# Optimization experiments

Measured on AMD Instinct MI355X. Metric: run time of the kernel, lower is better.

Reference implementation:

```python
import jax, jax.numpy as jnp
import numpy as np

N_NODES = 100000
N_EDGES = 1200000
N_FEAT = 128
HIDDEN = 64
N_GRAPHS = 256


def setup_inputs() -> dict:
    key = jax.random.key(0)
    ks = jax.random.split(key, 8)
    x = jax.random.normal(ks[0], (N_NODES, N_FEAT), dtype=jnp.float32)
    edge_index = jax.random.randint(ks[1], (2, N_EDGES), 0, N_NODES, dtype=jnp.int64)
    batch = jnp.sort(jax.random.randint(ks[2], (N_NODES,), 0, N_GRAPHS, dtype=jnp.int64))
    W1 = jax.random.normal(ks[3], (N_FEAT, HIDDEN), dtype=jnp.float32) * (1.0 / np.sqrt(N_FEAT))
    b1 = jnp.zeros((HIDDEN,), dtype=jnp.float32)
    W2 = jax.random.normal(ks[4], (HIDDEN, HIDDEN), dtype=jnp.float32) * (1.0 / np.sqrt(HIDDEN))
    b2 = jnp.zeros((HIDDEN,), dtype=jnp.float32)
    Wl = jax.random.normal(ks[5], (HIDDEN, 1), dtype=jnp.float32) * (1.0 / np.sqrt(HIDDEN))
    bl = jnp.zeros((1,), dtype=jnp.float32)
    return {"x": x, "edge_index": edge_index, "batch": batch,
            "W1": W1, "b1": b1, "W2": W2, "b2": b2, "Wl": Wl, "bl": bl}


def _gcn_conv(x, src, dst, W, b, n):
    # PyG GCNConv: linear transform, then sym-normalized scatter-add (self-loops already in src/dst)
    h = x @ W  # [N, out]
    deg = jax.ops.segment_sum(jnp.ones(src.shape[0], x.dtype), dst, num_segments=n)
    dinv = jnp.where(deg > 0, jax.lax.rsqrt(deg), jnp.zeros_like(deg))
    norm = dinv[src] * dinv[dst]  # [E+N]
    out = jax.ops.segment_sum(norm[:, None] * h[src], dst, num_segments=n)
    return out + b


def reference(x, edge_index, batch, W1, b1, W2, b2, Wl, bl):
    n = x.shape[0]
    loops = jnp.arange(n, dtype=edge_index.dtype)
    src = jnp.concatenate([edge_index[0], loops])
    dst = jnp.concatenate([edge_index[1], loops])
    h = _gcn_conv(x, src, dst, W1, b1, n)
    h = jax.nn.relu(h)
    h = _gcn_conv(h, src, dst, W2, b2, n)
    # global mean pool over graphs
    sums = jax.ops.segment_sum(h, batch, num_segments=N_GRAPHS)
    cnts = jax.ops.segment_sum(jnp.ones((n,), h.dtype), batch, num_segments=N_GRAPHS)
    pooled = sums / jnp.maximum(cnts, 1.0)[:, None]
    return pooled @ Wl + bl
```

## Files before the change

### kernel.cpp

```cpp
#include <hip/hip_runtime.h>

#define N_NODES 100000
#define N_EDGES 1200000
#define R_BUCKETS 256
#define RSZ 400
#define CAP 8192
#define CH 4096
#define NC 293

typedef _Float16 h8 __attribute__((ext_vector_type(8)));
typedef _Float16 h2 __attribute__((ext_vector_type(2)));
typedef float f32x16 __attribute__((ext_vector_type(16)));

__global__ __launch_bounds__(256) void bkt_scatter(const int* __restrict__ src,
                                                   const int* __restrict__ dst,
                                                   int* __restrict__ bucket_alloc,
                                                   int* __restrict__ ebuf, int E) {
    __shared__ int h[R_BUCKETS];
    __shared__ int off[R_BUCKETS];
    h[threadIdx.x] = 0;
    __syncthreads();
    int e0 = blockIdx.x * CH;
    int e1 = min(e0 + CH, E);
    for (int e = e0 + (int)threadIdx.x; e < e1; e += 256)
        atomicAdd(&h[dst[e] / RSZ], 1);
    __syncthreads();
    int b = threadIdx.x;
    int hc = h[b];
    off[b] = b * CAP + (hc > 0 ? atomicAdd(&bucket_alloc[b], hc) : 0);
    __syncthreads();
    for (int e = e0 + (int)threadIdx.x; e < e1; e += 256) {
        int d = dst[e];
        int bk = d / RSZ;
        int p = atomicAdd(&off[bk], 1);
        ebuf[p] = (src[e] << 9) | (d - bk * RSZ);
    }
}

__global__ __launch_bounds__(256) void bkt_build(const int* __restrict__ ebuf,
                                                 const int* __restrict__ bcnt,
                                                 int2* __restrict__ row2,
                                                 float* __restrict__ dinv,
                                                 int* __restrict__ csr, int N) {
    __shared__ int hist[RSZ];
    __shared__ int pref[RSZ];
    __shared__ int part[256];
    int r = blockIdx.x;
    int nbase = r * RSZ;
    int ebase = r * CAP;
    int ecnt = bcnt[r];
    for (int i = threadIdx.x; i < RSZ; i += 256) hist[i] = 0;
    __syncthreads();
    for (int e = (int)threadIdx.x; e < ecnt; e += 256)
        atomicAdd(&hist[ebuf[ebase + e] & 511], 1);
    __syncthreads();
    for (int i = threadIdx.x; i < RSZ; i += 256) {
        int gi = nbase + i;
        if (gi < N) dinv[gi] = rsqrtf((float)hist[i] + 1.0f);
    }
    int s0 = threadIdx.x * 2;
    int sum = (s0 < RSZ) ? hist[s0] + hist[s0 + 1] : 0;
    part[threadIdx.x] = sum;
    __syncthreads();
    for (int off = 1; off < 256; off <<= 1) {
        int v = (threadIdx.x >= off) ? part[threadIdx.x - off] : 0;
        __syncthreads();
        part[threadIdx.x] += v;
        __syncthreads();
    }
    if (s0 < RSZ) {
        int run = part[threadIdx.x] - sum;
        pref[s0] = run;
        pref[s0 + 1] = run + hist[s0];
    }
    __syncthreads();
    for (int i = threadIdx.x; i < RSZ; i += 256) {
        int gi = nbase + i;
        if (gi < N) row2[gi] = make_int2(ebase + pref[i], ebase + pref[i] + hist[i]);
    }
    __syncthreads();
    for (int e = (int)threadIdx.x; e < ecnt; e += 256) {
        int epk = ebuf[ebase + e];
        int t = atomicAdd(&pref[epk & 511], 1);
        csr[ebase + t] = (int)(((unsigned)epk) >> 9);
    }
}

__global__ void prep_kernel(const float* __restrict__ W1, const float* __restrict__ W2,
                            const float* __restrict__ Wl, float* __restrict__ w2l,
                            _Float16* __restrict__ whi, _Float16* __restrict__ wlo) {
    if (blockIdx.x == 32) {
        if (threadIdx.x < 64) {
            int f = threadIdx.x;
            float s = 0.0f;
            for (int o = 0; o < 64; o++) s += W2[f * 64 + o] * Wl[o];
            w2l[f] = s;
        }
        return;
    }
    int idx = blockIdx.x * 256 + threadIdx.x;
    int j = idx & 7;
    int lane = (idx >> 3) & 63;
    int kk = (idx >> 9) & 7;
    int nt = idx >> 12;
    int k = kk * 16 + (lane >> 5) * 8 + j;
    int n = nt * 32 + (lane & 31);
    float v = W1[k * 64 + n];
    _Float16 hi = (_Float16)v;
    whi[idx] = hi;
    wlo[idx] = (_Float16)(v - (float)hi);
}

__global__ __launch_bounds__(256) void gemm_mfma(const float* __restrict__ x,
                                                 const _Float16* __restrict__ whi,
                                                 const _Float16* __restrict__ wlo,
                                                 const float* __restrict__ dinv,
                                                 _Float16* __restrict__ out, int N) {
    int wave = threadIdx.x >> 6;
    int lane = threadIdx.x & 63;
    int base = blockIdx.x * 128 + wave * 32;
    int row = base + (lane & 31);
    int rowc = min(row, N - 1);
    const float* xrow = x + (size_t)rowc * 128 + (lane >> 5) * 8;

    f32x16 acc0, acc1;
#pragma unroll
    for (int i = 0; i < 16; i++) { acc0[i] = 0.f; acc1[i] = 0.f; }

#pragma unroll
    for (int kk = 0; kk < 8; kk++) {
        float4 xa = *reinterpret_cast<const float4*>(xrow + kk * 16);
        float4 xb = *reinterpret_cast<const float4*>(xrow + kk * 16 + 4);
        float xv[8] = {xa.x, xa.y, xa.z, xa.w, xb.x, xb.y, xb.z, xb.w};
        h8 ahi, alo;
#pragma unroll
        for (int j = 0; j < 8; j++) {
            _Float16 hi = (_Float16)xv[j];
            ahi[j] = hi;
            alo[j] = (_Float16)(xv[j] - (float)hi);
        }
        h8 b0h = *reinterpret_cast<const h8*>(whi + (size_t)(kk * 64 + lane) * 8);
        h8 b0l = *reinterpret_cast<const h8*>(wlo + (size_t)(kk * 64 + lane) * 8);
        h8 b1h = *reinterpret_cast<const h8*>(whi + (size_t)((8 + kk) * 64 + lane) * 8);
        h8 b1l = *reinterpret_cast<const h8*>(wlo + (size_t)((8 + kk) * 64 + lane) * 8);
        acc0 = __builtin_amdgcn_mfma_f32_32x32x16_f16(ahi, b0h, acc0, 0, 0, 0);
        acc0 = __builtin_amdgcn_mfma_f32_32x32x16_f16(ahi, b0l, acc0, 0, 0, 0);
        acc0 = __builtin_amdgcn_mfma_f32_32x32x16_f16(alo, b0h, acc0, 0, 0, 0);
        acc1 = __builtin_amdgcn_mfma_f32_32x32x16_f16(ahi, b1h, acc1, 0, 0, 0);
        acc1 = __builtin_amdgcn_mfma_f32_32x32x16_f16(ahi, b1l, acc1, 0, 0, 0);
        acc1 = __builtin_amdgcn_mfma_f32_32x32x16_f16(alo, b1h, acc1, 0, 0, 0);
    }

    int col = lane & 31;
    int rbase = base + 4 * (lane >> 5);
#pragma unroll
    for (int reg = 0; reg < 16; reg++) {
        int node = rbase + (reg & 3) + 8 * (reg >> 2);
        if (node < N) {
            float di = dinv[node];
            out[(size_t)node * 64 + col] = (_Float16)(di * acc0[reg]);
            out[(size_t)node * 64 + 32 + col] = (_Float16)(di * acc1[reg]);
        }
    }
}

#define AGG_NPB 32
__global__ __launch_bounds__(256) void agg1_kernel(const _Float16* __restrict__ t,
                                                   const int2* __restrict__ row2,
                                                   const int* __restrict__ csr,
                                                   const float* __restrict__ dinv,
                                                   const float* __restrict__ b1,
                                                   const float* __restrict__ w2l,
                                                   float* __restrict__ q, int N) {
    int lane = threadIdx.x & 63;
    int w = threadIdx.x >> 6;
    int hl = lane & 31;
    int hsel = lane >> 5;
    float2 b1v = reinterpret_cast<const float2*>(b1)[hl];
    float2 wlv = reinterpret_cast<const float2*>(w2l)[hl];
    int i0 = blockIdx.x * AGG_NPB;
    int iend = min(i0 + AGG_NPB, N);
    for (int ip = i0 + 2 * w; ip < iend; ip += 8) {
        int iA = ip;
        int iB = ip + 1;
        bool hasB = iB < iend;
        int2 rrA = row2[iA];
        int2 rrB = hasB ? row2[iB] : make_int2(rrA.x, rrA.x);
        int myi = hsel ? iB : iA;
        int myic = min(myi, N - 1);
        int rs = hsel ? rrB.x : rrA.x;
        int re = hsel ? rrB.y : rrA.y;
        int deg = re - rs;
        int kmax = max(rrA.y - rrA.x, rrB.y - rrB.x);
        int rlast = max(re - 1, rs);
        h2 sv = *reinterpret_cast<const h2*>(t + ((size_t)myic << 6) + (hl << 1));
        float a0 = (float)sv[0];
        float a1 = (float)sv[1];
        for (int base = 0; base < kmax; base += 32) {
            int sp = min(csr[min(rs + base + hl, rlast)] & 0x1FFFF, N - 1);
            int kend = min(kmax - base, 32);
            {
                h2 vv[16];
#pragma unroll
                for (int j = 0; j < 16; j++) {
                    int s = __shfl(sp, j, 32);
                    vv[j] = *reinterpret_cast<const h2*>(t + ((size_t)s << 6) + (hl << 1));
                }
#pragma unroll
                for (int j = 0; j < 16; j++) {
                    if (base + j < deg) {
                        a0 += (float)vv[j][0];
                        a1 += (float)vv[j][1];
                    }
                }
            }
            if (kend > 16) {
                h2 vv[16];
#pragma unroll
                for (int j = 0; j < 16; j++) {
                    int s = __shfl(sp, 16 + j, 32);
                    vv[j] = *reinterpret_cast<const h2*>(t + ((size_t)s << 6) + (hl << 1));
                }
#pragma unroll
                for (int j = 0; j < 16; j++) {
                    if (base + 16 + j < deg) {
                        a0 += (float)vv[j][0];
                        a1 += (float)vv[j][1];
                    }
                }
            }
        }
        float di = dinv[myic];
        float h0 = fmaxf(di * a0 + b1v.x, 0.f);
        float h1 = fmaxf(di * a1 + b1v.y, 0.f);
        float p = h0 * wlv.x + h1 * wlv.y;
        p += __shfl_xor(p, 1, 64);
        p += __shfl_xor(p, 2, 64);
        p += __shfl_xor(p, 4, 64);
        p += __shfl_xor(p, 8, 64);
        p += __shfl_xor(p, 16, 64);
        if (hl == 0 && myi < iend) q[myi] = di * p;
    }
}

__global__ __launch_bounds__(256) void agg2_pool_kernel(const float* __restrict__ q,
                                                        const int2* __restrict__ row2,
                                                        const int* __restrict__ csr,
                                                        const float* __restrict__ dinv,
                                                        const int* __restrict__ batch,
                                                        float* __restrict__ gsum,
                                                        float* __restrict__ gcnt, int N) {
    __shared__ float bins[256];
    __shared__ float cbins[256];
    bins[threadIdx.x] = 0.0f;
    cbins[threadIdx.x] = 0.0f;
    __syncthreads();
    int i = blockIdx.x * 256 + threadIdx.x;
    if (i < N) {
        int2 rr = row2[i];
        int rs = rr.x, re = rr.y;
        float acc = q[i];
        int rl = max(re - 1, rs);
        for (int j = rs; j < re; j += 4) {
            int e0 = csr[j];
            int e1 = csr[min(j + 1, rl)];
            int e2 = csr[min(j + 2, rl)];
            int e3 = csr[min(j + 3, rl)];
            float v0 = q[e0];
            float v1 = q[e1];
            float v2 = q[e2];
            float v3 = q[e3];
            acc += v0;
            if (j + 1 < re) acc += v1;
            if (j + 2 < re) acc += v2;
            if (j + 3 < re) acc += v3;
        }
        int g = batch[i];
        atomicAdd(&bins[g], dinv[i] * acc);
        atomicAdd(&cbins[g], 1.0f);
    }
    __syncthreads();
    int i0 = blockIdx.x * 256;
    if (i0 < N) {
        int ilast = min(i0 + 255, N - 1);
        int gmin = batch[i0];
        int gmax = batch[ilast];
        for (int g = gmin + (int)threadIdx.x; g <= gmax; g += 256) {
            atomicAdd(&gsum[g], bins[g]);
            atomicAdd(&gcnt[g], cbins[g]);
        }
    }
}

__global__ void out_kernel(const float* __restrict__ gsum, const float* __restrict__ gcnt,
                           const float* __restrict__ b2, const float* __restrict__ Wl,
                           const float* __restrict__ bl, float* __restrict__ out) {
    int g = threadIdx.x;
    int lane = g & 63;
    float c = b2[lane] * Wl[lane];
    c += __shfl_xor(c, 1, 64);
    c += __shfl_xor(c, 2, 64);
    c += __shfl_xor(c, 4, 64);
    c += __shfl_xor(c, 8, 64);
    c += __shfl_xor(c, 16, 64);
    c += __shfl_xor(c, 32, 64);
    out[g] = gsum[g] / fmaxf(gcnt[g], 1.0f) + c + bl[0];
}

extern "C" void kernel_launch(void* const* d_in, const int* in_sizes, int n_in,
                              void* d_out, int out_size, void* d_ws, size_t ws_size,
                              hipStream_t stream) {
    const float* x  = (const float*)d_in[0];
    const int*   ei = (const int*)d_in[1];
    const int*   batch = (const int*)d_in[2];
    const float* W1 = (const float*)d_in[3];
    const float* b1 = (const float*)d_in[4];
    const float* W2 = (const float*)d_in[5];
    const float* b2 = (const float*)d_in[6];
    const float* Wl = (const float*)d_in[7];
    const float* bl = (const float*)d_in[8];
    float* out = (float*)d_out;

    const int N = N_NODES, E = N_EDGES;
    const int nblk = (N + 255) / 256;
    const int* src = ei;
    const int* dst = ei + E;

    char* ws = (char*)d_ws;
    int*      ebuf      = (int*)ws;       ws += (size_t)R_BUCKETS * CAP * 4;
    int*      csr       = (int*)ws;       ws += (size_t)R_BUCKETS * CAP * 4;
    _Float16* buf1      = (_Float16*)ws;  ws += 6400000 * 2;
    int2*     row2      = (int2*)ws;      ws += 100096 * 8;
    float*    dinv      = (float*)ws;     ws += 100096 * 4;
    float*    q         = (float*)ws;     ws += 100096 * 4;
    float*    gsum      = (float*)ws;     ws += 256 * 4;
    int*      bucket_alloc = (int*)ws;    ws += 256 * 4;
    float*    gcnt      = (float*)ws;     ws += 256 * 4;
    float*    w2l       = (float*)ws;     ws += 256 * 4;
    _Float16* whi       = (_Float16*)ws;  ws += 8192 * 2;
    _Float16* wlo       = (_Float16*)ws;  ws += 8192 * 2;

    hipMemsetAsync(gsum, 0, 3072, stream);

    bkt_scatter<<<NC, 256, 0, stream>>>(src, dst, bucket_alloc, ebuf, E);
    bkt_build<<<R_BUCKETS, 256, 0, stream>>>(ebuf, bucket_alloc, row2, dinv, csr, N);

    prep_kernel<<<33, 256, 0, stream>>>(W1, W2, Wl, w2l, whi, wlo);

    gemm_mfma<<<(N + 127) / 128, 256, 0, stream>>>(x, whi, wlo, dinv, buf1, N);

    agg1_kernel<<<(N + AGG_NPB - 1) / AGG_NPB, 256, 0, stream>>>(
        buf1, row2, csr, dinv, b1, w2l, q, N);

    agg2_pool_kernel<<<nblk, 256, 0, stream>>>(q, row2, csr, dinv, batch, gsum, gcnt, N);

    out_kernel<<<1, 256, 0, stream>>>(gsum, gcnt, b2, Wl, bl, out);
}
```

Measured before the change: 201.7 us.

## Fuse degree counting, weight prep and output finalize into neighboring kernels

```diff
diff --git a/kernel.cpp b/kernel.cpp
--- a/kernel.cpp
+++ b/kernel.cpp
@@ -12,35 +12,67 @@
 typedef _Float16 h2 __attribute__((ext_vector_type(2)));
 typedef float f32x16 __attribute__((ext_vector_type(16)));
 
-__global__ __launch_bounds__(256) void bkt_scatter(const int* __restrict__ src,
-                                                   const int* __restrict__ dst,
-                                                   int* __restrict__ bucket_alloc,
-                                                   int* __restrict__ ebuf, int E) {
+__global__ __launch_bounds__(256) void scatter_deg_prep(const int* __restrict__ src,
+                                                        const int* __restrict__ dst,
+                                                        int* __restrict__ bucket_alloc,
+                                                        int* __restrict__ ebuf,
+                                                        int* __restrict__ deg,
+                                                        const float* __restrict__ W1,
+                                                        const float* __restrict__ W2,
+                                                        const float* __restrict__ Wl,
+                                                        float* __restrict__ w2l,
+                                                        _Float16* __restrict__ whi,
+                                                        _Float16* __restrict__ wlo, int E) {
     __shared__ int h[R_BUCKETS];
     __shared__ int off[R_BUCKETS];
+    __shared__ int dcache[CH];
     h[threadIdx.x] = 0;
     __syncthreads();
     int e0 = blockIdx.x * CH;
     int e1 = min(e0 + CH, E);
-    for (int e = e0 + (int)threadIdx.x; e < e1; e += 256)
-        atomicAdd(&h[dst[e] / RSZ], 1);
+    for (int e = e0 + (int)threadIdx.x; e < e1; e += 256) {
+        int d = dst[e];
+        dcache[e - e0] = d;
+        atomicAdd(&h[d / RSZ], 1);
+        atomicAdd(&deg[d], 1);
+    }
     __syncthreads();
     int b = threadIdx.x;
     int hc = h[b];
     off[b] = b * CAP + (hc > 0 ? atomicAdd(&bucket_alloc[b], hc) : 0);
     __syncthreads();
     for (int e = e0 + (int)threadIdx.x; e < e1; e += 256) {
-        int d = dst[e];
+        int d = dcache[e - e0];
         int bk = d / RSZ;
         int p = atomicAdd(&off[bk], 1);
         ebuf[p] = (src[e] << 9) | (d - bk * RSZ);
     }
+    if (blockIdx.x == 32) {
+        if (threadIdx.x < 64) {
+            int f = threadIdx.x;
+            float s = 0.0f;
+            for (int o = 0; o < 64; o++) s += W2[f * 64 + o] * Wl[o];
+            w2l[f] = s;
+        }
+    } else if (blockIdx.x < 32) {
+        int idx = blockIdx.x * 256 + threadIdx.x;
+        int j = idx & 7;
+        int lane = (idx >> 3) & 63;
+        int kk = (idx >> 9) & 7;
+        int nt = idx >> 12;
+        int k = kk * 16 + (lane >> 5) * 8 + j;
+        int n = nt * 32 + (lane & 31);
+        float v = W1[k * 64 + n];
+        _Float16 hi = (_Float16)v;
+        whi[idx] = hi;
+        wlo[idx] = (_Float16)(v - (float)hi);
+    }
 }
 
 __global__ __launch_bounds__(256) void bkt_build(const int* __restrict__ ebuf,
                                                  const int* __restrict__ bcnt,
+                                                 const int* __restrict__ deg,
                                                  int2* __restrict__ row2,
-                                                 float* __restrict__ dinv,
                                                  int* __restrict__ csr, int N) {
     __shared__ int hist[RSZ];
     __shared__ int pref[RSZ];
@@ -49,15 +81,11 @@
     int nbase = r * RSZ;
     int ebase = r * CAP;
     int ecnt = bcnt[r];
-    for (int i = threadIdx.x; i < RSZ; i += 256) hist[i] = 0;
-    __syncthreads();
-    for (int e = (int)threadIdx.x; e < ecnt; e += 256)
-        atomicAdd(&hist[ebuf[ebase + e] & 511], 1);
-    __syncthreads();
     for (int i = threadIdx.x; i < RSZ; i += 256) {
         int gi = nbase + i;
-        if (gi < N) dinv[gi] = rsqrtf((float)hist[i] + 1.0f);
-    }
+        hist[i] = (gi < N) ? deg[gi] : 0;
+    }
+    __syncthreads();
     int s0 = threadIdx.x * 2;
     int sum = (s0 < RSZ) ? hist[s0] + hist[s0 + 1] : 0;
     part[threadIdx.x] = sum;
@@ -86,35 +114,10 @@
     }
 }
 
-__global__ void prep_kernel(const float* __restrict__ W1, const float* __restrict__ W2,
-                            const float* __restrict__ Wl, float* __restrict__ w2l,
-                            _Float16* __restrict__ whi, _Float16* __restrict__ wlo) {
-    if (blockIdx.x == 32) {
-        if (threadIdx.x < 64) {
-            int f = threadIdx.x;
-            float s = 0.0f;
-            for (int o = 0; o < 64; o++) s += W2[f * 64 + o] * Wl[o];
-            w2l[f] = s;
-        }
-        return;
-    }
-    int idx = blockIdx.x * 256 + threadIdx.x;
-    int j = idx & 7;
-    int lane = (idx >> 3) & 63;
-    int kk = (idx >> 9) & 7;
-    int nt = idx >> 12;
-    int k = kk * 16 + (lane >> 5) * 8 + j;
-    int n = nt * 32 + (lane & 31);
-    float v = W1[k * 64 + n];
-    _Float16 hi = (_Float16)v;
-    whi[idx] = hi;
-    wlo[idx] = (_Float16)(v - (float)hi);
-}
-
 __global__ __launch_bounds__(256) void gemm_mfma(const float* __restrict__ x,
                                                  const _Float16* __restrict__ whi,
                                                  const _Float16* __restrict__ wlo,
-                                                 const float* __restrict__ dinv,
+                                                 const int* __restrict__ deg,
                                                  _Float16* __restrict__ out, int N) {
     int wave = threadIdx.x >> 6;
     int lane = threadIdx.x & 63;
@@ -157,7 +160,7 @@
     for (int reg = 0; reg < 16; reg++) {
         int node = rbase + (reg & 3) + 8 * (reg >> 2);
         if (node < N) {
-            float di = dinv[node];
+            float di = rsqrtf((float)deg[node] + 1.0f);
             out[(size_t)node * 64 + col] = (_Float16)(di * acc0[reg]);
             out[(size_t)node * 64 + 32 + col] = (_Float16)(di * acc1[reg]);
         }
@@ -168,7 +171,7 @@
 __global__ __launch_bounds__(256) void agg1_kernel(const _Float16* __restrict__ t,
                                                    const int2* __restrict__ row2,
                                                    const int* __restrict__ csr,
-                                                   const float* __restrict__ dinv,
+                                                   const int* __restrict__ deg,
                                                    const float* __restrict__ b1,
                                                    const float* __restrict__ w2l,
                                                    float* __restrict__ q, int N) {
@@ -190,7 +193,7 @@
         int myic = min(myi, N - 1);
         int rs = hsel ? rrB.x : rrA.x;
         int re = hsel ? rrB.y : rrA.y;
-        int deg = re - rs;
+        int dg = re - rs;
         int kmax = max(rrA.y - rrA.x, rrB.y - rrB.x);
         int rlast = max(re - 1, rs);
         h2 sv = *reinterpret_cast<const h2*>(t + ((size_t)myic << 6) + (hl << 1));
@@ -208,7 +211,7 @@
                 }
 #pragma unroll
                 for (int j = 0; j < 16; j++) {
-                    if (base + j < deg) {
+                    if (base + j < dg) {
                         a0 += (float)vv[j][0];
                         a1 += (float)vv[j][1];
                     }
@@ -223,14 +226,14 @@
                 }
 #pragma unroll
                 for (int j = 0; j < 16; j++) {
-                    if (base + 16 + j < deg) {
+                    if (base + 16 + j < dg) {
                         a0 += (float)vv[j][0];
                         a1 += (float)vv[j][1];
                     }
                 }
             }
         }
-        float di = dinv[myic];
+        float di = rsqrtf((float)deg[myic] + 1.0f);
         float h0 = fmaxf(di * a0 + b1v.x, 0.f);
         float h1 = fmaxf(di * a1 + b1v.y, 0.f);
         float p = h0 * wlv.x + h1 * wlv.y;
@@ -243,15 +246,22 @@
     }
 }
 
+#define NBLK2 391
 __global__ __launch_bounds__(256) void agg2_pool_kernel(const float* __restrict__ q,
                                                         const int2* __restrict__ row2,
                                                         const int* __restrict__ csr,
-                                                        const float* __restrict__ dinv,
+                                                        const int* __restrict__ deg,
                                                         const int* __restrict__ batch,
                                                         float* __restrict__ gsum,
-                                                        float* __restrict__ gcnt, int N) {
+                                                        float* __restrict__ gcnt,
+                                                        int* __restrict__ done,
+                                                        const float* __restrict__ b2,
+                                                        const float* __restrict__ Wl,
+                                                        const float* __restrict__ bl,
+                                                        float* __restrict__ out, int N) {
     __shared__ float bins[256];
     __shared__ float cbins[256];
+    __shared__ int lastflag;
     bins[threadIdx.x] = 0.0f;
     cbins[threadIdx.x] = 0.0f;
     __syncthreads();
@@ -276,7 +286,7 @@
             if (j + 3 < re) acc += v3;
         }
         int g = batch[i];
-        atomicAdd(&bins[g], dinv[i] * acc);
+        atomicAdd(&bins[g], rsqrtf((float)deg[i] + 1.0f) * acc);
         atomicAdd(&cbins[g], 1.0f);
     }
     __syncthreads();
@@ -290,21 +300,25 @@
             atomicAdd(&gcnt[g], cbins[g]);
         }
     }
-}
-
-__global__ void out_kernel(const float* __restrict__ gsum, const float* __restrict__ gcnt,
-                           const float* __restrict__ b2, const float* __restrict__ Wl,
-                           const float* __restrict__ bl, float* __restrict__ out) {
-    int g = threadIdx.x;
-    int lane = g & 63;
-    float c = b2[lane] * Wl[lane];
-    c += __shfl_xor(c, 1, 64);
-    c += __shfl_xor(c, 2, 64);
-    c += __shfl_xor(c, 4, 64);
-    c += __shfl_xor(c, 8, 64);
-    c += __shfl_xor(c, 16, 64);
-    c += __shfl_xor(c, 32, 64);
-    out[g] = gsum[g] / fmaxf(gcnt[g], 1.0f) + c + bl[0];
+    __threadfence();
+    __syncthreads();
+    if (threadIdx.x == 0) lastflag = (atomicAdd(done, 1) == NBLK2 - 1) ? 1 : 0;
+    __syncthreads();
+    if (lastflag) {
+        __threadfence();
+        int g = threadIdx.x;
+        int lane = g & 63;
+        float c = b2[lane] * Wl[lane];
+        c += __shfl_xor(c, 1, 64);
+        c += __shfl_xor(c, 2, 64);
+        c += __shfl_xor(c, 4, 64);
+        c += __shfl_xor(c, 8, 64);
+        c += __shfl_xor(c, 16, 64);
+        c += __shfl_xor(c, 32, 64);
+        float s = atomicAdd(&gsum[g], 0.0f);
+        float cn = atomicAdd(&gcnt[g], 0.0f);
+        out[g] = s / fmaxf(cn, 1.0f) + c + bl[0];
+    }
 }
 
 extern "C" void kernel_launch(void* const* d_in, const int* in_sizes, int n_in,
@@ -322,7 +336,6 @@
     float* out = (float*)d_out;
 
     const int N = N_NODES, E = N_EDGES;
-    const int nblk = (N + 255) / 256;
     const int* src = ei;
     const int* dst = ei + E;
 
@@ -331,28 +344,28 @@
     int*      csr       = (int*)ws;       ws += (size_t)R_BUCKETS * CAP * 4;
     _Float16* buf1      = (_Float16*)ws;  ws += 6400000 * 2;
     int2*     row2      = (int2*)ws;      ws += 100096 * 8;
-    float*    dinv      = (float*)ws;     ws += 100096 * 4;
+    int*      deg       = (int*)ws;       ws += 100096 * 4;
+    float*    gsum      = (float*)ws;     ws += 256 * 4;
+    float*    gcnt      = (float*)ws;     ws += 256 * 4;
+    int*      bucket_alloc = (int*)ws;    ws += 256 * 4;
+    int*      done      = (int*)ws;       ws += 256 * 4;
     float*    q         = (float*)ws;     ws += 100096 * 4;
-    float*    gsum      = (float*)ws;     ws += 256 * 4;
-    int*      bucket_alloc = (int*)ws;    ws += 256 * 4;
-    float*    gcnt      = (float*)ws;     ws += 256 * 4;
     float*    w2l       = (float*)ws;     ws += 256 * 4;
     _Float16* whi       = (_Float16*)ws;  ws += 8192 * 2;
     _Float16* wlo       = (_Float16*)ws;  ws += 8192 * 2;
 
-    hipMemsetAsync(gsum, 0, 3072, stream);
-
-    bkt_scatter<<<NC, 256, 0, stream>>>(src, dst, bucket_alloc, ebuf, E);
-    bkt_build<<<R_BUCKETS, 256, 0, stream>>>(ebuf, bucket_alloc, row2, dinv, csr, N);
-
-    prep_kernel<<<33, 256, 0, stream>>>(W1, W2, Wl, w2l, whi, wlo);
-
-    gemm_mfma<<<(N + 127) / 128, 256, 0, stream>>>(x, whi, wlo, dinv, buf1, N);
+    hipMemsetAsync(deg, 0, 400384 + 4096, stream);
+
+    scatter_deg_prep<<<NC, 256, 0, stream>>>(src, dst, bucket_alloc, ebuf, deg,
+                                             W1, W2, Wl, w2l, whi, wlo, E);
+
+    bkt_build<<<R_BUCKETS, 256, 0, stream>>>(ebuf, bucket_alloc, deg, row2, csr, N);
+
+    gemm_mfma<<<(N + 127) / 128, 256, 0, stream>>>(x, whi, wlo, deg, buf1, N);
 
     agg1_kernel<<<(N + AGG_NPB - 1) / AGG_NPB, 256, 0, stream>>>(
-        buf1, row2, csr, dinv, b1, w2l, q, N);
-
-    agg2_pool_kernel<<<nblk, 256, 0, stream>>>(q, row2, csr, dinv, batch, gsum, gcnt, N);
-
-    out_kernel<<<1, 256, 0, stream>>>(gsum, gcnt, b2, Wl, bl, out);
-}
+        buf1, row2, csr, deg, b1, w2l, q, N);
+
+    agg2_pool_kernel<<<NBLK2, 256, 0, stream>>>(q, row2, csr, deg, batch,
+                                                gsum, gcnt, done, b2, Wl, bl, out, N);
+}
```

Measured after the change: 255.3 us. 26.6% more time.
